# Kernel tuning notes

Hardware: AMD Instinct MI355X
Metric: run time of the kernel (lower is better)

## Reference

```python
import jax, jax.numpy as jnp
import numpy as np

B, T, D = 2, 2048, 1024
H = 16
DH = D // H


def setup_inputs() -> dict:
    key = jax.random.key(0)
    ks = jax.random.split(key, 6)
    s = 1.0 / np.sqrt(D)
    return {
        "input_emb": jax.random.normal(ks[0], (B, T, D), dtype=jnp.float32),
        "W_key": jax.random.normal(ks[1], (D, D), dtype=jnp.float32) * s,
        "W_query": jax.random.normal(ks[2], (D, D), dtype=jnp.float32) * s,
        "W_value": jax.random.normal(ks[3], (D, D), dtype=jnp.float32) * s,
        "W_out": jax.random.normal(ks[4], (D, D), dtype=jnp.float32) * s,
        "b_out": jnp.zeros((D,), dtype=jnp.float32),
    }


def reference(input_emb, W_key, W_query, W_value, W_out, b_out):
    b, t, _ = input_emb.shape
    # projections (no bias on K/Q/V, matching bias_on=False)
    k = (input_emb @ W_key).reshape(b, t, H, DH).transpose(0, 2, 1, 3)    # [b,h,t,dh]
    q = (input_emb @ W_query).reshape(b, t, H, DH).transpose(0, 2, 1, 3)
    v = (input_emb @ W_value).reshape(b, t, H, DH).transpose(0, 2, 1, 3)
    # NOTE: source computes K @ Q^T (not Q @ K^T) — reproduce faithfully.
    scores = jnp.einsum("bhid,bhjd->bhij", k, q) / jnp.sqrt(jnp.float32(DH))
    mask = jnp.triu(jnp.ones((t, t), dtype=bool), k=1)                    # True where j > i
    scores = jnp.where(mask, -jnp.inf, scores)
    attn = jax.nn.softmax(scores, axis=-1)                                # softmax over j (query axis)
    ctx = jnp.einsum("bhij,bhjd->bhid", attn, v)                          # [b,h,t,dh]
    ctx = ctx.transpose(0, 2, 1, 3).reshape(b, t, H * DH)                 # [b,t,d]
    return ctx @ W_out + b_out
```

## Files before the change

### kernel.cpp

```cpp
#include <hip/hip_runtime.h>
#include <cstdint>
#include <cstddef>

#define T_SEQ 2048
#define DMODEL 1024
#define NHEAD 16
#define DHEAD 64
#define BATCH 2
#define MROWS (BATCH * T_SEQ)

typedef __attribute__((ext_vector_type(8))) short bf16x8;
typedef __attribute__((ext_vector_type(4))) float f32x4;
typedef unsigned int u32;

__device__ __forceinline__ unsigned short f2bf(float f) {
  u32 u = __float_as_uint(f);
  u32 r = (u + 0x7FFFu + ((u >> 16) & 1u)) >> 16;
  return (unsigned short)r;
}

__device__ __forceinline__ u32 cvtpk(float a, float b) {
  u32 r;
  asm("v_cvt_pk_bf16_f32 %0, %1, %2" : "=v"(r) : "v"(a), "v"(b));
  return r;
}

__device__ __forceinline__ void gl_lds16(const unsigned short* g, unsigned short* l) {
  __builtin_amdgcn_global_load_lds(
      (const __attribute__((address_space(1))) u32*)g,
      (__attribute__((address_space(3))) u32*)l, 16, 0, 0);
}

__global__ void k_prep(const float* __restrict__ X, unsigned short* __restrict__ Xb,
                       const float* __restrict__ W0, const float* __restrict__ W1,
                       const float* __restrict__ W2, const float* __restrict__ W3,
                       unsigned short* __restrict__ T0, unsigned short* __restrict__ T1,
                       unsigned short* __restrict__ T2, unsigned short* __restrict__ T3) {
  const int bid = blockIdx.x;
  if (bid < 4096) {
    int i = (bid * 256 + threadIdx.x) * 4;
    float4 v = *reinterpret_cast<const float4*>(X + i);
    ushort4 o;
    o.x = f2bf(v.x); o.y = f2bf(v.y); o.z = f2bf(v.z); o.w = f2bf(v.w);
    *reinterpret_cast<ushort4*>(Xb + i) = o;
    return;
  }
  const int b2 = bid - 4096;
  const int z = b2 >> 10;
  const int rem = b2 & 1023;
  const int cx = rem & 31, ry = rem >> 5;
  const float* W = (z == 0) ? W0 : (z == 1) ? W1 : (z == 2) ? W2 : W3;
  unsigned short* Wt = (z == 0) ? T0 : (z == 1) ? T1 : (z == 2) ? T2 : T3;
  __shared__ float tile[32][33];
  const int c0 = cx * 32, r0 = ry * 32;
  const int tx = threadIdx.x & 31, ty = threadIdx.x >> 5;
#pragma unroll
  for (int i = ty; i < 32; i += 8)
    tile[i][tx] = W[(size_t)(r0 + i) * DMODEL + c0 + tx];
  __syncthreads();
#pragma unroll
  for (int i = ty; i < 32; i += 8)
    Wt[(size_t)(c0 + i) * DMODEL + r0 + tx] = f2bf(tile[tx][i]);
}

__global__ __launch_bounds__(256, 2)
void k_gemm_qkv(const unsigned short* __restrict__ Xb,
                const unsigned short* __restrict__ Wkt,
                const unsigned short* __restrict__ Wqt,
                const unsigned short* __restrict__ Wvt,
                unsigned short* __restrict__ Qr,
                unsigned short* __restrict__ Kr,
                unsigned short* __restrict__ Vt)
{
  __shared__ __align__(16) unsigned short As[2][128 * 32];
  __shared__ __align__(16) unsigned short Bs[2][128 * 32];
  const int orig = blockIdx.x;
  const int t = (orig & 7) * 96 + (orig >> 3);
  const int z = t >> 8;
  const int remt = t & 255;
  const int by = remt >> 3, bx = remt & 7;
  const unsigned short* Bt = (z == 0) ? Wkt : (z == 1) ? Wqt : Wvt;

  const int tid = threadIdx.x;
  const int lane = tid & 63, w = tid >> 6;
  const int wr = w >> 1, wc = w & 1;
  const int l15 = lane & 15, l4 = lane >> 4;
  const int m0 = by * 128, n0 = bx * 128;

  const int srow = tid >> 2, scc = tid & 3;
  const unsigned short* Ab0 = Xb + (size_t)(m0 + srow) * DMODEL + scc * 8;
  const unsigned short* Bb0 = Bt + (size_t)(n0 + srow) * DMODEL + scc * 8;
  const unsigned short* Ab1 = Ab0 + (size_t)64 * DMODEL;
  const unsigned short* Bb1 = Bb0 + (size_t)64 * DMODEL;

#define GSTAGE(buf, k0)                                                   \
  {                                                                       \
    gl_lds16(Ab0 + (k0), As[buf] + tid * 8);                              \
    gl_lds16(Ab1 + (k0), As[buf] + 2048 + tid * 8);                       \
    gl_lds16(Bb0 + (k0), Bs[buf] + tid * 8);                              \
    gl_lds16(Bb1 + (k0), Bs[buf] + 2048 + tid * 8);                       \
  }

#define GCOMP(buf)                                                        \
  {                                                                       \
    bf16x8 af[4], bfr[4];                                                 \
    _Pragma("unroll")                                                     \
    for (int mi = 0; mi < 4; ++mi)                                        \
      af[mi] = *reinterpret_cast<const bf16x8*>(As[buf] + (wr * 64 + mi * 16 + l15) * 32 + l4 * 8); \
    _Pragma("unroll")                                                     \
    for (int ni = 0; ni < 4; ++ni)                                        \
      bfr[ni] = *reinterpret_cast<const bf16x8*>(Bs[buf] + (wc * 64 + ni * 16 + l15) * 32 + l4 * 8); \
    __builtin_amdgcn_s_setprio(1);                                        \
    _Pragma("unroll")                                                     \
    for (int mi = 0; mi < 4; ++mi)                                        \
      _Pragma("unroll")                                                   \
      for (int ni = 0; ni < 4; ++ni)                                      \
        acc[mi][ni] = __builtin_amdgcn_mfma_f32_16x16x32_bf16(af[mi], bfr[ni], acc[mi][ni], 0, 0, 0); \
    __builtin_amdgcn_s_setprio(0);                                        \
  }

#define GSYNC                                                             \
  __builtin_amdgcn_sched_barrier(0);                                      \
  asm volatile("s_waitcnt vmcnt(0)" ::: "memory");                        \
  __builtin_amdgcn_s_barrier();                                           \
  __builtin_amdgcn_sched_barrier(0);

  f32x4 acc[4][4] = {};

  GSTAGE(0, 0)
  GSYNC
  for (int k0 = 0; k0 < DMODEL; k0 += 64) {
    GSTAGE(1, k0 + 32)
    GCOMP(0)
    GSYNC
    if (k0 + 64 < DMODEL) { GSTAGE(0, k0 + 64) }
    GCOMP(1)
    GSYNC
  }
#undef GSTAGE
#undef GCOMP
#undef GSYNC

  if (z < 2) {
    unsigned short* C = (z == 0) ? Qr : Kr;
#pragma unroll
    for (int mi = 0; mi < 4; ++mi)
#pragma unroll
      for (int ni = 0; ni < 4; ++ni) {
        const int col = n0 + wc * 64 + ni * 16 + l15;
        const int rowb = m0 + wr * 64 + mi * 16 + l4 * 4;
#pragma unroll
        for (int r = 0; r < 4; ++r)
          C[(size_t)(rowb + r) * DMODEL + col] = f2bf(acc[mi][ni][r]);
      }
  } else {
#pragma unroll
    for (int mi = 0; mi < 4; ++mi)
#pragma unroll
      for (int ni = 0; ni < 4; ++ni) {
        const int col = n0 + wc * 64 + ni * 16 + l15;
        const int h = col >> 6, dh = col & 63;
        const int rowb = m0 + wr * 64 + mi * 16 + l4 * 4;
        const int b = rowb >> 11, tt = rowb & (T_SEQ - 1);
        const int tl = tt & 63;
        const int tp = (tt & ~63) | (tl & 32) | ((tl & 12) << 1) | ((tl & 16) >> 2);
        unsigned short* p = Vt + ((size_t)(b * NHEAD + h) * DHEAD + dh) * T_SEQ + tp;
        ushort4 pkv;
        pkv.x = f2bf(acc[mi][ni][0]); pkv.y = f2bf(acc[mi][ni][1]);
        pkv.z = f2bf(acc[mi][ni][2]); pkv.w = f2bf(acc[mi][ni][3]);
        *reinterpret_cast<ushort4*>(p) = pkv;
      }
  }
}

__global__ __launch_bounds__(256, 2)
void k_attn(const unsigned short* __restrict__ Qr,
            const unsigned short* __restrict__ Kr,
            const unsigned short* __restrict__ Vp,
            unsigned short* __restrict__ ctx)
{
  __shared__ __align__(16) char lds[65536];
  const int tid = threadIdx.x;
  const int lane = tid & 63, w = tid >> 6;
  const int l15 = lane & 15, l4 = lane >> 4;

  const int x = blockIdx.x;
  const int xcd = x & 7, idx = x >> 3;
  const int bh = xcd + 8 * (idx & 3);
  const int cpair = idx >> 2;
  const int b = bh >> 4, h = bh & 15;

  const unsigned short* Qbase = Qr + (size_t)b * T_SEQ * DMODEL + h * DHEAD;
  const unsigned short* Kbase = Kr + (size_t)b * T_SEQ * DMODEL + h * DHEAD;
  const unsigned short* Vbase = Vp + (size_t)bh * DHEAD * T_SEQ;
  unsigned short* obase = ctx + (size_t)b * T_SEQ * DMODEL + h * DHEAD;

  const float SC = 0.18033688011112042f;
  const float M0 = 12.0f;
  const int srow = tid >> 3, scb = tid & 7;
  const int scolE = (scb ^ (srow & 7)) << 3;

  const int sw = (l15 & 7) << 4;
  const char* aK0 = lds + l15 * 128 + ((l4 * 16) ^ sw);
  const char* aK1 = lds + l15 * 128 + (((64 + l4 * 16)) ^ sw);

  const unsigned short* kp = Kbase + (size_t)srow * DMODEL + scolE;
  const unsigned short* vpb = Vbase + (size_t)srow * T_SEQ + scolE;

#define KRD(P, st, ni, v1) (*reinterpret_cast<const bf16x8*>(((v1) ? aK1 : aK0) + (P) * 16384 + (st) * 8192 + (ni) * 2048))
#define VRD(P, st, df, hk) (*reinterpret_cast<const bf16x8*>(((hk) ? aK1 : aK0) + 32768 + (P) * 16384 + (st) * 8192 + (df) * 2048))

#define STAGE(KD, VD, kg, vg)                                                     \
      {                                                                           \
        gl_lds16((kg), (KD) + tid * 8);                                           \
        gl_lds16((kg) + 32 * DMODEL, (KD) + 2048 + tid * 8);                      \
        gl_lds16((kg) + 64 * DMODEL, (KD) + 4096 + tid * 8);                      \
        gl_lds16((kg) + 96 * DMODEL, (KD) + 6144 + tid * 8);                      \
        gl_lds16((vg), (VD) + tid * 8);                                           \
        gl_lds16((vg) + 32 * T_SEQ, (VD) + 2048 + tid * 8);                       \
        gl_lds16((vg) + 64, (VD) + 4096 + tid * 8);                               \
        gl_lds16((vg) + 32 * T_SEQ + 64, (VD) + 6144 + tid * 8);                  \
      }

#define GROUP_BODY(g, P)                                                          \
    {                                                                             \
      const int kv0 = (g) * 128;                                                  \
      const bool diag = ((g) == NG - 1);                                          \
      __builtin_amdgcn_sched_barrier(0);                                          \
      asm volatile("s_waitcnt vmcnt(0)" ::: "memory");                            \
      __builtin_amdgcn_sched_barrier(0);                                          \
      __builtin_amdgcn_s_barrier();                                               \
      __builtin_amdgcn_sched_barrier(0);                                          \
      if ((g) + 1 < NG) {                                                         \
        unsigned short* Kn = (unsigned short*)(lds + ((P) ^ 1) * 16384);          \
        unsigned short* Vn = (unsigned short*)(lds + 32768 + ((P) ^ 1) * 16384);  \
        STAGE(Kn, Vn, kstage, vstage)                                             \
        kstage += 128 * DMODEL; vstage += 128;                                    \
      }                                                                           \
      __builtin_amdgcn_sched_barrier(0);                                          \
      const bool a1 = !diag || codd;                                              \
      const int nlim0 = (diag && !codd) ? (w + 1) : 4;                            \
      const int nlim1 = (diag && codd) ? (w + 1) : 4;                             \
      f32x4 S[2][4] = {};                                                         \
      __builtin_amdgcn_s_setprio(1);                                              \
      _Pragma("unroll")                                                           \
      for (int ni = 0; ni < 4; ++ni)                                              \
        if (ni < nlim0) {                                                         \
          S[0][ni] = __builtin_amdgcn_mfma_f32_16x16x32_bf16(KRD(P, 0, ni, 0), qf[0], S[0][ni], 0, 0, 0); \
          S[0][ni] = __builtin_amdgcn_mfma_f32_16x16x32_bf16(KRD(P, 0, ni, 1), qf[1], S[0][ni], 0, 0, 0); \
        }                                                                         \
      if (a1) {                                                                   \
        _Pragma("unroll")                                                         \
        for (int ni = 0; ni < 4; ++ni)                                            \
          if (ni < nlim1) {                                                       \
            S[1][ni] = __builtin_amdgcn_mfma_f32_16x16x32_bf16(KRD(P, 1, ni, 0), qf[0], S[1][ni], 0, 0, 0); \
            S[1][ni] = __builtin_amdgcn_mfma_f32_16x16x32_bf16(KRD(P, 1, ni, 1), qf[1], S[1][ni], 0, 0, 0); \
          }                                                                       \
      }                                                                           \
      __builtin_amdgcn_s_setprio(0);                                              \
      if (diag) {                                                                 \
        if (!codd) {                                                              \
          _Pragma("unroll")                                                       \
          for (int ni = 0; ni < 4; ++ni)                                          \
            if (ni < nlim0) {                                                     \
              _Pragma("unroll")                                                   \
              for (int r = 0; r < 4; ++r)                                         \
                if (kv0 + ni * 16 + l4 * 4 + r > qrow) S[0][ni][r] = -INFINITY;   \
            }                                                                     \
        } else {                                                                  \
          _Pragma("unroll")                                                       \
          for (int ni = 0; ni < 4; ++ni)                                          \
            if (ni < nlim1) {                                                     \
              _Pragma("unroll")                                                   \
              for (int r = 0; r < 4; ++r)                                         \
                if (kv0 + 64 + ni * 16 + l4 * 4 + r > qrow) S[1][ni][r] = -INFINITY; \
            }                                                                     \
        }                                                                         \
      }                                                                           \
      union __align__(16) PW { u32 u[2][2][4]; bf16x8 v[2][2]; } pw = {};         \
      _Pragma("unroll")                                                           \
      for (int ni = 0; ni < 4; ++ni)                                              \
        if (ni < nlim0) {                                                         \
          const float p0 = __builtin_amdgcn_exp2f(__builtin_fmaf(S[0][ni][0], SC, -M0)); \
          const float p1 = __builtin_amdgcn_exp2f(__builtin_fmaf(S[0][ni][1], SC, -M0)); \
          const float p2 = __builtin_amdgcn_exp2f(__builtin_fmaf(S[0][ni][2], SC, -M0)); \
          const float p3 = __builtin_amdgcn_exp2f(__builtin_fmaf(S[0][ni][3], SC, -M0)); \
          lP += (p0 + p1) + (p2 + p3);                                            \
          pw.u[0][ni >> 1][(ni & 1) * 2]     = cvtpk(p0, p1);                     \
          pw.u[0][ni >> 1][(ni & 1) * 2 + 1] = cvtpk(p2, p3);                     \
        }                                                                         \
      if (a1) {                                                                   \
        _Pragma("unroll")                                                         \
        for (int ni = 0; ni < 4; ++ni)                                            \
          if (ni < nlim1) {                                                       \
            const float p0 = __builtin_amdgcn_exp2f(__builtin_fmaf(S[1][ni][0], SC, -M0)); \
            const float p1 = __builtin_amdgcn_exp2f(__builtin_fmaf(S[1][ni][1], SC, -M0)); \
            const float p2 = __builtin_amdgcn_exp2f(__builtin_fmaf(S[1][ni][2], SC, -M0)); \
            const float p3 = __builtin_amdgcn_exp2f(__builtin_fmaf(S[1][ni][3], SC, -M0)); \
            lP += (p0 + p1) + (p2 + p3);                                          \
            pw.u[1][ni >> 1][(ni & 1) * 2]     = cvtpk(p0, p1);                   \
            pw.u[1][ni >> 1][(ni & 1) * 2 + 1] = cvtpk(p2, p3);                   \
          }                                                                       \
      }                                                                           \
      __builtin_amdgcn_s_setprio(1);                                              \
      {                                                                           \
        const int hkl0 = (diag && !codd) ? ((nlim0 + 1) >> 1) : 2;                \
        _Pragma("unroll")                                                         \
        for (int hk = 0; hk < 2; ++hk)                                            \
          if (hk < hkl0) {                                                        \
            _Pragma("unroll")                                                     \
            for (int df = 0; df < 4; ++df)                                        \
              O[df] = __builtin_amdgcn_mfma_f32_16x16x32_bf16(VRD(P, 0, df, hk), pw.v[0][hk], O[df], 0, 0, 0); \
          }                                                                       \
      }                                                                           \
      if (a1) {                                                                   \
        const int hkl1 = (diag && codd) ? ((nlim1 + 1) >> 1) : 2;                 \
        _Pragma("unroll")                                                         \
        for (int hk = 0; hk < 2; ++hk)                                            \
          if (hk < hkl1) {                                                        \
            _Pragma("unroll")                                                     \
            for (int df = 0; df < 4; ++df)                                        \
              O[df] = __builtin_amdgcn_mfma_f32_16x16x32_bf16(VRD(P, 1, df, hk), pw.v[1][hk], O[df], 0, 0, 0); \
          }                                                                       \
      }                                                                           \
      __builtin_amdgcn_s_setprio(0);                                              \
      __builtin_amdgcn_sched_barrier(0);                                          \
    }

  for (int half = 0; half < 2; ++half) {
    const int c = half ? (31 - cpair) : cpair;
    const bool codd = (c & 1) != 0;
    const int q0w = c * 64 + w * 16;
    const int NG = (c + 2) >> 1;
    const int qrow = q0w + l15;

    bf16x8 qf[2];
#pragma unroll
    for (int ks = 0; ks < 2; ++ks)
      qf[ks] = *reinterpret_cast<const bf16x8*>(
          Qbase + (size_t)(q0w + l15) * DMODEL + ks * 32 + l4 * 8);

    __builtin_amdgcn_sched_barrier(0);
    __builtin_amdgcn_s_barrier();
    __builtin_amdgcn_sched_barrier(0);
    {
      unsigned short* Ks = (unsigned short*)(lds);
      unsigned short* Vs = (unsigned short*)(lds + 32768);
      STAGE(Ks, Vs, kp, vpb)
    }
    const unsigned short* kstage = kp + 128 * DMODEL;
    const unsigned short* vstage = vpb + 128;

    f32x4 O[4] = {};
    float lP = 0.f;

    for (int g2 = 0; g2 < NG; g2 += 2) {
      GROUP_BODY(g2, 0)
      if (g2 + 1 < NG) GROUP_BODY(g2 + 1, 1)
    }

    float lS = lP;
    lS += __shfl_xor(lS, 16);
    lS += __shfl_xor(lS, 32);
    const float rinv = 1.0f / lS;
#pragma unroll
    for (int df = 0; df < 4; ++df) {
      ushort4 o;
      o.x = f2bf(O[df][0] * rinv);
      o.y = f2bf(O[df][1] * rinv);
      o.z = f2bf(O[df][2] * rinv);
      o.w = f2bf(O[df][3] * rinv);
      *reinterpret_cast<ushort4*>(obase + (size_t)qrow * DMODEL + df * 16 + l4 * 4) = o;
    }
  }
#undef GROUP_BODY
#undef STAGE
#undef KRD
#undef VRD
}

__global__ __launch_bounds__(256, 2)
void k_gemm_out(const unsigned short* __restrict__ Ab,
                const unsigned short* __restrict__ Bt,
                const float* __restrict__ bias,
                float* __restrict__ C)
{
  __shared__ __align__(16) unsigned short As[2][128 * 32];
  __shared__ __align__(16) unsigned short Bs[2][128 * 32];
  const int orig = blockIdx.x;
  const int t = (orig & 7) * 32 + (orig >> 3);
  const int by = t >> 3, bx = t & 7;

  const int tid = threadIdx.x;
  const int lane = tid & 63, w = tid >> 6;
  const int wr = w >> 1, wc = w & 1;
  const int l15 = lane & 15, l4 = lane >> 4;
  const int m0 = by * 128, n0 = bx * 128;

  const int srow = tid >> 2, scc = tid & 3;
  const unsigned short* Ab0 = Ab + (size_t)(m0 + srow) * DMODEL + scc * 8;
  const unsigned short* Bb0 = Bt + (size_t)(n0 + srow) * DMODEL + scc * 8;
  const unsigned short* Ab1 = Ab0 + (size_t)64 * DMODEL;
  const unsigned short* Bb1 = Bb0 + (size_t)64 * DMODEL;

#define GSTAGE(buf, k0)                                                   \
  {                                                                       \
    gl_lds16(Ab0 + (k0), As[buf] + tid * 8);                              \
    gl_lds16(Ab1 + (k0), As[buf] + 2048 + tid * 8);                       \
    gl_lds16(Bb0 + (k0), Bs[buf] + tid * 8);                              \
    gl_lds16(Bb1 + (k0), Bs[buf] + 2048 + tid * 8);                       \
  }

#define GCOMP(buf)                                                        \
  {                                                                       \
    bf16x8 af[4], bfr[4];                                                 \
    _Pragma("unroll")                                                     \
    for (int mi = 0; mi < 4; ++mi)                                        \
      af[mi] = *reinterpret_cast<const bf16x8*>(As[buf] + (wr * 64 + mi * 16 + l15) * 32 + l4 * 8); \
    _Pragma("unroll")                                                     \
    for (int ni = 0; ni < 4; ++ni)                                        \
      bfr[ni] = *reinterpret_cast<const bf16x8*>(Bs[buf] + (wc * 64 + ni * 16 + l15) * 32 + l4 * 8); \
    __builtin_amdgcn_s_setprio(1);                                        \
    _Pragma("unroll")                                                     \
    for (int mi = 0; mi < 4; ++mi)                                        \
      _Pragma("unroll")                                                   \
      for (int ni = 0; ni < 4; ++ni)                                      \
        acc[mi][ni] = __builtin_amdgcn_mfma_f32_16x16x32_bf16(af[mi], bfr[ni], acc[mi][ni], 0, 0, 0); \
    __builtin_amdgcn_s_setprio(0);                                        \
  }

#define GSYNC                                                             \
  __builtin_amdgcn_sched_barrier(0);                                      \
  asm volatile("s_waitcnt vmcnt(0)" ::: "memory");                        \
  __builtin_amdgcn_s_barrier();                                           \
  __builtin_amdgcn_sched_barrier(0);

  f32x4 acc[4][4] = {};

  GSTAGE(0, 0)
  GSYNC
  for (int k0 = 0; k0 < DMODEL; k0 += 64) {
    GSTAGE(1, k0 + 32)
    GCOMP(0)
    GSYNC
    if (k0 + 64 < DMODEL) { GSTAGE(0, k0 + 64) }
    GCOMP(1)
    GSYNC
  }
#undef GSTAGE
#undef GCOMP
#undef GSYNC

#pragma unroll
  for (int mi = 0; mi < 4; ++mi)
#pragma unroll
    for (int ni = 0; ni < 4; ++ni) {
      const int col = n0 + wc * 64 + ni * 16 + l15;
      const float bv = bias[col];
      const int rowb = m0 + wr * 64 + mi * 16 + l4 * 4;
#pragma unroll
      for (int r = 0; r < 4; ++r)
        C[(size_t)(rowb + r) * DMODEL + col] = acc[mi][ni][r] + bv;
    }
}

extern "C" void kernel_launch(void* const* d_in, const int* in_sizes, int n_in,
                              void* d_out, int out_size, void* d_ws, size_t ws_size,
                              hipStream_t stream) {
  const float* X  = (const float*)d_in[0];
  const float* Wk = (const float*)d_in[1];
  const float* Wq = (const float*)d_in[2];
  const float* Wv = (const float*)d_in[3];
  const float* Wo = (const float*)d_in[4];
  const float* bo = (const float*)d_in[5];
  float* out = (float*)d_out;

  char* ws = (char*)d_ws;
  const size_t MB = 1024 * 1024;
  unsigned short* Xb  = (unsigned short*)(ws + 0 * MB);
  unsigned short* Wkt = (unsigned short*)(ws + 8 * MB);
  unsigned short* Wqt = (unsigned short*)(ws + 10 * MB);
  unsigned short* Wvt = (unsigned short*)(ws + 12 * MB);
  unsigned short* Wot = (unsigned short*)(ws + 14 * MB);
  unsigned short* Qr  = (unsigned short*)(ws + 16 * MB);
  unsigned short* Kr  = (unsigned short*)(ws + 24 * MB);
  unsigned short* Vt  = (unsigned short*)(ws + 32 * MB);
  unsigned short* Ctx = (unsigned short*)(ws + 40 * MB);

  k_prep<<<8192, 256, 0, stream>>>(X, Xb, Wk, Wq, Wv, Wo, Wkt, Wqt, Wvt, Wot);
  k_gemm_qkv<<<768, 256, 0, stream>>>(Xb, Wkt, Wqt, Wvt, Qr, Kr, Vt);
  k_attn<<<dim3(512), 256, 0, stream>>>(Qr, Kr, Vt, Ctx);
  k_gemm_out<<<256, 256, 0, stream>>>(Ctx, Wot, bo, out);
}
```

Baseline: 102.7 us.

## Triple-buffer LDS in QKV and output GEMMs with partial vmcnt waits

Both projection GEMM kernels move from a double-buffered LDS pipeline with full vmcnt(0) waits to a three-stage ring buffer. Each step waits only until the older stage's loads have landed (vmcnt(4)), leaving the newest prefetch in flight. It then issues the next prefetch and computes, with one barrier per 32-wide k step. This keeps global loads in flight during compute and trades extra LDS (48KB per block) for deeper prefetch, which may reduce occupancy at two blocks per CU.

```diff
diff --git a/kernel.cpp b/kernel.cpp
--- a/kernel.cpp
+++ b/kernel.cpp
@@ -72,8 +72,8 @@
                 unsigned short* __restrict__ Kr,
                 unsigned short* __restrict__ Vt)
 {
-  __shared__ __align__(16) unsigned short As[2][128 * 32];
-  __shared__ __align__(16) unsigned short Bs[2][128 * 32];
+  __shared__ __align__(16) unsigned short As[3][128 * 32];
+  __shared__ __align__(16) unsigned short Bs[3][128 * 32];
   const int orig = blockIdx.x;
   const int t = (orig & 7) * 96 + (orig >> 3);
   const int z = t >> 8;
@@ -93,12 +93,12 @@
   const unsigned short* Ab1 = Ab0 + (size_t)64 * DMODEL;
   const unsigned short* Bb1 = Bb0 + (size_t)64 * DMODEL;
 
-#define GSTAGE(buf, k0)                                                   \
+#define GSTAGE(buf, koff)                                                 \
   {                                                                       \
-    gl_lds16(Ab0 + (k0), As[buf] + tid * 8);                              \
-    gl_lds16(Ab1 + (k0), As[buf] + 2048 + tid * 8);                       \
-    gl_lds16(Bb0 + (k0), Bs[buf] + tid * 8);                              \
-    gl_lds16(Bb1 + (k0), Bs[buf] + 2048 + tid * 8);                       \
+    gl_lds16(Ab0 + (koff), As[buf] + tid * 8);                            \
+    gl_lds16(Ab1 + (koff), As[buf] + 2048 + tid * 8);                     \
+    gl_lds16(Bb0 + (koff), Bs[buf] + tid * 8);                            \
+    gl_lds16(Bb1 + (koff), Bs[buf] + 2048 + tid * 8);                     \
   }
 
 #define GCOMP(buf)                                                        \
@@ -119,27 +119,34 @@
     __builtin_amdgcn_s_setprio(0);                                        \
   }
 
-#define GSYNC                                                             \
-  __builtin_amdgcn_sched_barrier(0);                                      \
-  asm volatile("s_waitcnt vmcnt(0)" ::: "memory");                        \
-  __builtin_amdgcn_s_barrier();                                           \
-  __builtin_amdgcn_sched_barrier(0);
+#define SB __builtin_amdgcn_sched_barrier(0);
+#define GW4 asm volatile("s_waitcnt vmcnt(4)" ::: "memory");
+#define GW0 asm volatile("s_waitcnt vmcnt(0)" ::: "memory");
+
+#define GSTEP(P, NB)                                                      \
+  SB GW4 SB __builtin_amdgcn_s_barrier(); SB                              \
+  if (ko < DMODEL) { GSTAGE(NB, ko) ko += 32; }                           \
+  GCOMP(P)
 
   f32x4 acc[4][4] = {};
 
   GSTAGE(0, 0)
-  GSYNC
-  for (int k0 = 0; k0 < DMODEL; k0 += 64) {
-    GSTAGE(1, k0 + 32)
-    GCOMP(0)
-    GSYNC
-    if (k0 + 64 < DMODEL) { GSTAGE(0, k0 + 64) }
-    GCOMP(1)
-    GSYNC
-  }
+  GSTAGE(1, 32)
+  int ko = 64;
+  for (int j = 0; j < 10; ++j) {
+    GSTEP(0, 2)
+    GSTEP(1, 0)
+    GSTEP(2, 1)
+  }
+  SB GW4 SB __builtin_amdgcn_s_barrier(); SB
+  GCOMP(0)
+  SB GW0 SB __builtin_amdgcn_s_barrier(); SB
+  GCOMP(1)
+#undef GSTEP
 #undef GSTAGE
 #undef GCOMP
-#undef GSYNC
+#undef GW4
+#undef GW0
 
   if (z < 2) {
     unsigned short* C = (z == 0) ? Qr : Kr;
@@ -385,8 +392,8 @@
                 const float* __restrict__ bias,
                 float* __restrict__ C)
 {
-  __shared__ __align__(16) unsigned short As[2][128 * 32];
-  __shared__ __align__(16) unsigned short Bs[2][128 * 32];
+  __shared__ __align__(16) unsigned short As[3][128 * 32];
+  __shared__ __align__(16) unsigned short Bs[3][128 * 32];
   const int orig = blockIdx.x;
   const int t = (orig & 7) * 32 + (orig >> 3);
   const int by = t >> 3, bx = t & 7;
@@ -403,12 +410,12 @@
   const unsigned short* Ab1 = Ab0 + (size_t)64 * DMODEL;
   const unsigned short* Bb1 = Bb0 + (size_t)64 * DMODEL;
 
-#define GSTAGE(buf, k0)                                                   \
+#define GSTAGE(buf, koff)                                                 \
   {                                                                       \
-    gl_lds16(Ab0 + (k0), As[buf] + tid * 8);                              \
-    gl_lds16(Ab1 + (k0), As[buf] + 2048 + tid * 8);                       \
-    gl_lds16(Bb0 + (k0), Bs[buf] + tid * 8);                              \
-    gl_lds16(Bb1 + (k0), Bs[buf] + 2048 + tid * 8);                       \
+    gl_lds16(Ab0 + (koff), As[buf] + tid * 8);                            \
+    gl_lds16(Ab1 + (koff), As[buf] + 2048 + tid * 8);                     \
+    gl_lds16(Bb0 + (koff), Bs[buf] + tid * 8);                            \
+    gl_lds16(Bb1 + (koff), Bs[buf] + 2048 + tid * 8);                     \
   }
 
 #define GCOMP(buf)                                                        \
@@ -429,27 +436,34 @@
     __builtin_amdgcn_s_setprio(0);                                        \
   }
 
-#define GSYNC                                                             \
-  __builtin_amdgcn_sched_barrier(0);                                      \
-  asm volatile("s_waitcnt vmcnt(0)" ::: "memory");                        \
-  __builtin_amdgcn_s_barrier();                                           \
-  __builtin_amdgcn_sched_barrier(0);
+#define GW4 asm volatile("s_waitcnt vmcnt(4)" ::: "memory");
+#define GW0 asm volatile("s_waitcnt vmcnt(0)" ::: "memory");
+
+#define GSTEP(P, NB)                                                      \
+  SB GW4 SB __builtin_amdgcn_s_barrier(); SB                              \
+  if (ko < DMODEL) { GSTAGE(NB, ko) ko += 32; }                           \
+  GCOMP(P)
 
   f32x4 acc[4][4] = {};
 
   GSTAGE(0, 0)
-  GSYNC
-  for (int k0 = 0; k0 < DMODEL; k0 += 64) {
-    GSTAGE(1, k0 + 32)
-    GCOMP(0)
-    GSYNC
-    if (k0 + 64 < DMODEL) { GSTAGE(0, k0 + 64) }
-    GCOMP(1)
-    GSYNC
-  }
+  GSTAGE(1, 32)
+  int ko = 64;
+  for (int j = 0; j < 10; ++j) {
+    GSTEP(0, 2)
+    GSTEP(1, 0)
+    GSTEP(2, 1)
+  }
+  SB GW4 SB __builtin_amdgcn_s_barrier(); SB
+  GCOMP(0)
+  SB GW0 SB __builtin_amdgcn_s_barrier(); SB
+  GCOMP(1)
+#undef GSTEP
 #undef GSTAGE
 #undef GCOMP
-#undef GSYNC
+#undef GW4
+#undef GW0
+#undef SB
 
 #pragma unroll
   for (int mi = 0; mi < 4; ++mi)
```

Result: no change. 102.7 us (+0.1%).
